# Performance work log

Hardware: AMD Instinct MI355X
Metric: run time of the kernel (lower is better)

The kernel has to match this reference:

```python
import jax, jax.numpy as jnp
import numpy as np

B, S, D, H = 8, 1024, 768, 12
HEAD_DIM = D // H  # 64
# NOTE: original code divides scores by scaling=(head_dim)**-0.5, i.e. MULTIPLIES by sqrt(head_dim)
SCORE_SCALE = float(HEAD_DIM) ** 0.5


def setup_inputs() -> dict:
    key = jax.random.key(0)
    ks = jax.random.split(key, 9)
    std = 1.0 / np.sqrt(D)
    return {
        "x":  jax.random.normal(ks[0], (B, S, D), jnp.float32),
        "Wq": jax.random.normal(ks[1], (H, D, D), jnp.float32) * std,
        "bq": jax.random.normal(ks[2], (H, D), jnp.float32) * std,
        "Wk": jax.random.normal(ks[3], (H, D, D), jnp.float32) * std,
        "bk": jax.random.normal(ks[4], (H, D), jnp.float32) * std,
        "Wv": jax.random.normal(ks[5], (H, D, D), jnp.float32) * std,
        "bv": jax.random.normal(ks[6], (H, D), jnp.float32) * std,
        "Wp": jax.random.normal(ks[7], (H * D, D), jnp.float32) * (1.0 / np.sqrt(H * D)),
        "bp": jax.random.normal(ks[8], (D,), jnp.float32) * std,
    }


def reference(x, Wq, bq, Wk, bk, Wv, bv, Wp, bp):
    # Per-head full-width projections, batched over the head axis h.
    q = jnp.einsum('bsd,hde->bhse', x, Wq) + bq[None, :, None, :]  # [B,H,S,D]
    k = jnp.einsum('bsd,hde->bhse', x, Wk) + bk[None, :, None, :]
    v = jnp.einsum('bsd,hde->bhse', x, Wv) + bv[None, :, None, :]
    scores = jnp.einsum('bhse,bhte->bhst', q, k) * SCORE_SCALE    # [B,H,S,S]
    attn = jax.nn.softmax(scores, axis=-1)
    o = jnp.einsum('bhst,bhte->bhse', attn, v)                     # [B,H,S,D]
    # concat heads along last dim (head-major order matches torch.cat)
    o = jnp.transpose(o, (0, 2, 1, 3)).reshape(B, S, H * D)        # [B,S,H*D]
    return o @ Wp + bp                                             # [B,S,D]
```

## Files before the change

### kernel.cpp

```cpp
#include <hip/hip_runtime.h>


typedef __attribute__((ext_vector_type(8))) short bf16x8;
typedef __attribute__((ext_vector_type(4))) float fx4;

#define NB 8
#define NS 1024
#define ND 768
#define NH 12

__device__ __forceinline__ unsigned short f2bf(float x) {
    unsigned int u = __float_as_uint(x);
    u += 0x7fffu + ((u >> 16) & 1u);
    return (unsigned short)(u >> 16);
}
__device__ __forceinline__ float bf2f(unsigned short h) {
    return __uint_as_float(((unsigned int)h) << 16);
}

__device__ __forceinline__ void gll16(const void* g, void* l) {
    __builtin_amdgcn_global_load_lds(
        (const __attribute__((address_space(1))) void*)g,
        (__attribute__((address_space(3))) void*)l, 16, 0, 0);
}

__device__ __forceinline__ void split_body(const float* __restrict__ in,
                                           unsigned short* __restrict__ hi,
                                           unsigned short* __restrict__ lo, int i) {
    float4 v = ((const float4*)in)[i];
    ushort4 h, l;
    h.x = f2bf(v.x); l.x = f2bf(v.x - bf2f(h.x));
    h.y = f2bf(v.y); l.y = f2bf(v.y - bf2f(h.y));
    h.z = f2bf(v.z); l.z = f2bf(v.z - bf2f(h.z));
    h.w = f2bf(v.w); l.w = f2bf(v.w - bf2f(h.w));
    ((ushort4*)hi)[i] = h;
    ((ushort4*)lo)[i] = l;
}

template<int NTERMS, class Epi>
__device__ __forceinline__ void gemm_core(
    char* __restrict__ smem,
    const unsigned short* __restrict__ Ah, const unsigned short* __restrict__ Al, int lda,
    const unsigned short* __restrict__ Bh, const unsigned short* __restrict__ Bl, int ldb,
    int K, Epi epi)
{
    constexpr int TILE = 16384;

    const int t = threadIdx.x;
    const int lane = t & 63;
    const int w = t >> 6;
    const int wm = (w >> 1) << 6;
    const int wn = (w & 1) << 6;
    const int lr = lane & 15;
    const int lg = lane >> 4;

    const int l3 = lane >> 3;
    const int cs = (lane & 7) ^ l3;
    const int ldsw = w << 12;

    const long gsA = (long)(w * 32 + l3) * lda * 2 + cs * 16;
    const long gsB = (long)(w * 32 + l3) * ldb * 2 + cs * 16;
    const long giA = (long)lda * 16;
    const long giB = (long)ldb * 16;

    const char* pAh = (const char*)Ah;
    const char* pBh = (const char*)Bh;
    const char* pAl = (const char*)Al;
    const char* pBl = (const char*)Bl;
    char* smA  = smem;
    char* smB  = smem + TILE;
    char* smA2 = smem + ((NTERMS == 3) ? 2 * TILE : 0);
    char* smB2 = smem + ((NTERMS == 3) ? 3 * TILE : TILE);

// ... 30 lines not shown
            for (int i = 0; i < 4; i++) {
                fa[i] = *(const bf16x8*)((const unsigned short*)smA + rowA[i] + pc);
                fb[i] = *(const bf16x8*)((const unsigned short*)smB + rowB[i] + pc);
            }
            if constexpr (NTERMS == 3) {
                #pragma unroll
                for (int i = 0; i < 4; i++) {
                    fa2[i] = *(const bf16x8*)((const unsigned short*)smA2 + rowA[i] + pc);
                    fb2[i] = *(const bf16x8*)((const unsigned short*)smB2 + rowB[i] + pc);
                }
            }
            #pragma unroll
            for (int i = 0; i < 4; i++)
                #pragma unroll
                for (int j = 0; j < 4; j++) {
                    acc[i][j] = __builtin_amdgcn_mfma_f32_16x16x32_bf16(fa[i], fb[j], acc[i][j], 0, 0, 0);
                    if constexpr (NTERMS == 3) {
                        acc[i][j] = __builtin_amdgcn_mfma_f32_16x16x32_bf16(fa[i], fb2[j], acc[i][j], 0, 0, 0);
                        acc[i][j] = __builtin_amdgcn_mfma_f32_16x16x32_bf16(fa2[i], fb[j], acc[i][j], 0, 0, 0);
                    }
                }
        }
    }

    #pragma unroll
    for (int i = 0; i < 4; i++)
        #pragma unroll
        for (int j = 0; j < 4; j++)
            #pragma unroll
            for (int r = 0; r < 4; r++)
                epi(wm + (i << 4) + (lg << 2) + r, wn + (j << 4) + lr, acc[i][j][r]);
}

__device__ __forceinline__ void softmax_rows(float* __restrict__ Sc, int blk) {
    int row = blk * 4 + ((int)threadIdx.x >> 6);
    int lane = threadIdx.x & 63;
    float* rp = Sc + (long)row * NS;
    const float4* src = (const float4*)rp + (lane << 2);
    float v[16];
    #pragma unroll
    for (int i = 0; i < 4; i++) {
        float4 a = src[i];
        v[i * 4 + 0] = a.x; v[i * 4 + 1] = a.y; v[i * 4 + 2] = a.z; v[i * 4 + 3] = a.w;
    }
    float m = v[0];
    #pragma unroll
    for (int i = 1; i < 16; i++) m = fmaxf(m, v[i]);
    #pragma unroll
    for (int o = 32; o > 0; o >>= 1) m = fmaxf(m, __shfl_xor(m, o));
    float s = 0.f, p[16];
    #pragma unroll
    for (int i = 0; i < 16; i++) { p[i] = __expf((v[i] - m) * 8.0f); s += p[i]; }
    #pragma unroll
    for (int o = 32; o > 0; o >>= 1) s += __shfl_xor(s, o);
    float inv = 1.0f / s;
    unsigned int wrd[8];
    #pragma unroll
    for (int i = 0; i < 8; i++) {
        unsigned int u0 = f2bf(p[2 * i] * inv);
        unsigned int u1 = f2bf(p[2 * i + 1] * inv);
        wrd[i] = u0 | (u1 << 16);
    }
    uint4* dst = (uint4*)((unsigned short*)rp + (lane << 4));
    dst[0] = make_uint4(wrd[0], wrd[1], wrd[2], wrd[3]);
    dst[1] = make_uint4(wrd[4], wrd[5], wrd[6], wrd[7]);
}

__global__ void k_setup1(
    const float* __restrict__ x, unsigned short* __restrict__ xh, unsigned short* __restrict__ xl,
    const float* __restrict__ Wq, unsigned short* __restrict__ Wqh, unsigned short* __restrict__ Wql,
    const float* __restrict__ Wk, unsigned short* __restrict__ Wkh, unsigned short* __restrict__ Wkl,
    const float* __restrict__ bq, float* __restrict__ rk)
{
    const int bx = blockIdx.x;
    if (bx < 6144) {
        split_body(x, xh, xl, bx * 256 + threadIdx.x);
    } else if (bx < 13056) {
        split_body(Wq, Wqh, Wql, (bx - 6144) * 256 + threadIdx.x);
    } else if (bx < 19968) {
        split_body(Wk, Wkh, Wkl, (bx - 13056) * 256 + threadIdx.x);
    } else {
        const int idx = bx - 19968;
        const int h = idx / 192;
        const int d = (idx % 192) * 4 + ((int)threadIdx.x >> 6);
        const int lane = threadIdx.x & 63;
        const float4* row = (const float4*)(Wk + ((long)h * ND + d) * ND);
        const float4* bv4 = (const float4*)(bq + h * ND);
        float acc = 0.f;
        #pragma unroll
        for (int i = 0; i < 3; i++) {
            float4 a = row[lane + (i << 6)];
            float4 b = bv4[lane + (i << 6)];
            acc += a.x * b.x + a.y * b.y + a.z * b.z + a.w * b.w;
        }
        #pragma unroll
        for (int o = 32; o > 0; o >>= 1) acc += __shfl_xor(acc, o);
        if (lane == 0) rk[h * ND + d] = acc;
    }
}

__global__ __launch_bounds__(256, 2) void k_setup2(
    const unsigned short* __restrict__ Wkh, const unsigned short* __restrict__ Wkl,
    const unsigned short* __restrict__ Wqh, const unsigned short* __restrict__ Wql,
    unsigned short* __restrict__ MTh, unsigned short* __restrict__ MTl,
    const float* __restrict__ x, const float* __restrict__ rk, float* __restrict__ w_all)
{
    __shared__ __align__(16) char smem[65536];
    const int bx = blockIdx.x;
    if (bx < 432) {
        const int tid = (bx & 7) * 54 + (bx >> 3);
        const int n0 = (tid % 6) << 7;
        const int m0 = ((tid / 6) % 6) << 7;
        const long hw = (long)(tid / 36) * (ND * ND);
        unsigned short* oh = MTh + hw + (long)m0 * ND + n0;
        unsigned short* ol = MTl + hw + (long)m0 * ND + n0;
        gemm_core<3>(smem, Wkh + hw + (long)m0 * ND, Wkl + hw + (long)m0 * ND, ND,
                     Wqh + hw + (long)n0 * ND, Wql + hw + (long)n0 * ND, ND, ND,
                     [=](int r, int c, float v) {
                         unsigned short hh = f2bf(v);
                         oh[r * ND + c] = hh;
                         ol[r * ND + c] = f2bf(v - bf2f(hh));
                     });
    } else {
        float* srk = (float*)smem;
        for (int i = threadIdx.x; i < NH * ND; i += 256) srk[i] = rk[i];
        __syncthreads();
        const int row = (bx - 432) * 4 + ((int)threadIdx.x >> 6);
        const int lane = threadIdx.x & 63;
        const float4* xr = (const float4*)(x + (long)row * ND);
        float4 xa[3];
        #pragma unroll
        for (int i = 0; i < 3; i++) xa[i] = xr[lane + (i << 6)];
        for (int h = 0; h < NH; h++) {
            const float* r = srk + h * ND;
            float acc = 0.f;
            #pragma unroll
            for (int i = 0; i < 3; i++) {
                int e = (lane + (i << 6)) << 2;
                acc += xa[i].x * r[e] + xa[i].y * r[e + 1]
                     + xa[i].z * r[e + 2] + xa[i].w * r[e + 3];
            }
            #pragma unroll
            for (int o = 32; o > 0; o >>= 1) acc += __shfl_xor(acc, o);
            if (lane == 0) w_all[h * (NB * NS) + row] = acc;
        }
    }
}

__global__ void k_setup3(const float* __restrict__ Wv, unsigned short* __restrict__ Wvb,
                         const float* __restrict__ Wp, unsigned short* __restrict__ WpT)
{
    __shared__ float tile[64][65];
    const int bx = blockIdx.x;
    if (bx < 6912) {
        int i = bx * 256 + threadIdx.x;
        float4 v = ((const float4*)Wv)[i];
        ushort4 h;
        h.x = f2bf(v.x); h.y = f2bf(v.y); h.z = f2bf(v.z); h.w = f2bf(v.w);
        ((ushort4*)Wvb)[i] = h;
    } else {
        const int idx = bx - 6912;
        const int c0 = (idx % 12) * 64;
        const int r0 = ((idx / 12) % 12) * 64;
        const long zo = (long)(idx / 144) * (ND * ND);
        const float* in = Wp + zo;
        unsigned short* oh = WpT + zo;
        const int tc = threadIdx.x & 63, t4 = threadIdx.x >> 6;
        #pragma unroll
        for (int i = 0; i < 16; i++) {
            int r = (i << 2) + t4;
            tile[r][tc] = in[(long)(r0 + r) * ND + c0 + tc];
        }
        __syncthreads();
        #pragma unroll
        for (int i = 0; i < 16; i++) {
            int c = (i << 2) + t4;
            oh[(long)(c0 + c) * ND + r0 + tc] = f2bf(tile[tc][c]);
        }
    }
}

__global__ __launch_bounds__(256, 2) void k_setup4(
    const unsigned short* __restrict__ WpT, const unsigned short* __restrict__ Wvb,
    unsigned short* __restrict__ NTo, const float* __restrict__ bv,
    float* __restrict__ s_all)
{
    __shared__ __align__(16) char smem[32768];
    const int bx = blockIdx.x;
    if (bx < 432) {
        const int tid = (bx & 7) * 54 + (bx >> 3);
        const int n0 = (tid % 6) << 7;
        const int m0 = ((tid / 6) % 6) << 7;
        const long hw = (long)(tid / 36) * (ND * ND);
        unsigned short* o = NTo + hw + (long)m0 * ND + n0;
        gemm_core<1>(smem, WpT + hw + (long)m0 * ND, nullptr, ND,
                     Wvb + hw + (long)n0 * ND, nullptr, ND, ND,
                     [=](int r, int c, float v) { o[r * ND + c] = f2bf(v); });
    } else {
        const int idx = bx - 432;
        const int h = idx / 192;
        const int j = (idx % 192) * 4 + ((int)threadIdx.x >> 6);
        const int lane = threadIdx.x & 63;
        const ushort4* row = (const ushort4*)(WpT + ((long)h * ND + j) * ND);
        const float* bvh = bv + h * ND;
        float acc = 0.f;
        #pragma unroll
        for (int i = 0; i < 3; i++) {
            int c = lane + (i << 6);
            ushort4 u = row[c];
            int e = c << 2;
            acc += bf2f(u.x) * bvh[e] + bf2f(u.y) * bvh[e + 1]
                 + bf2f(u.z) * bvh[e + 2] + bf2f(u.w) * bvh[e + 3];
        }
        #pragma unroll
        for (int o = 32; o > 0; o >>= 1) acc += __shfl_xor(acc, o);
        if (lane == 0) s_all[h * ND + j] = acc;
    }
}


__global__ __launch_bounds__(256, 2) void k_G0(
    const unsigned short* __restrict__ xh, const unsigned short* __restrict__ xl,
    const unsigned short* __restrict__ MTh, const unsigned short* __restrict__ MTl,
    unsigned short* __restrict__ Gh, unsigned short* __restrict__ Gl)
{
    __shared__ __align__(16) char smem[65536];
    const int bx = blockIdx.x;
    const int xcd = bx & 7, idx = bx >> 3;
    const int m0 = (xcd * 8 + idx / 6) << 7;
    const int n0 = (idx % 6) << 7;
    unsigned short* oh = Gh + (long)m0 * ND + n0;
    unsigned short* ol = Gl + (long)m0 * ND + n0;
    gemm_core<3>(smem, xh + (long)m0 * ND, xl + (long)m0 * ND, ND,
                 MTh + (long)n0 * ND, MTl + (long)n0 * ND, ND, ND,
                 [=](int r, int c, float v) {
                     unsigned short hh = f2bf(v);
                     oh[(long)r * ND + c] = hh;
                     ol[(long)r * ND + c] = f2bf(v - bf2f(hh));
                 });
}

__global__ __launch_bounds__(256, 2) void k_SZ(
    const unsigned short* __restrict__ Gh, const unsigned short* __restrict__ Gl,
    const unsigned short* __restrict__ xh, const unsigned short* __restrict__ xl,
    const float* __restrict__ wv, float* __restrict__ Sc,
    const unsigned short* __restrict__ NTh, const float* __restrict__ sh,
    unsigned short* __restrict__ ZT)
{
    __shared__ __align__(16) char smem[65536];
    const int bx = blockIdx.x;
    if (bx < 512) {
        const int bl = bx & 7, idx = bx >> 3;
        const int m0 = (idx >> 3) << 7;
        const int n0 = (idx & 7) << 7;
        const long ao = ((long)bl * NS + m0) * ND;
        const long bo = ((long)bl * NS + n0) * ND;
        const float* ww = wv + bl * NS + n0;
        float* out = Sc + ((long)bl * NS + m0) * NS + n0;
        gemm_core<3>(smem, Gh + ao, Gl + ao, ND, xh + bo, xl + bo, ND, ND,
                     [=](int r, int c, float v) { out[(long)r * NS + c] = v + ww[c]; });
    } else {
        const int g = bx - 512;
        const int xcd = g & 7, idx = g >> 3;
        const int m0 = (xcd * 8 + idx / 6) << 7;
        const int n0 = (idx % 6) << 7;
        const int bl = m0 >> 10;
        const int s0 = m0 & (NS - 1);
        unsigned short* zt = ZT + (long)bl * (ND * NS);
        gemm_core<1>(smem, xh + (long)m0 * ND, nullptr, ND,
                     NTh + (long)n0 * ND, nullptr, ND, ND,
                     [=](int r, int c, float v) {
                         zt[(long)(n0 + c) * NS + s0 + r] = f2bf(v + sh[n0 + c]);
                     });
    }
}

__global__ __launch_bounds__(256) void k_SM(float* __restrict__ Sc) {
    softmax_rows(Sc, blockIdx.x);
}

template<int MODE>
__global__ __launch_bounds__(256, 2) void k_PVG(
    const unsigned short* __restrict__ P, const unsigned short* __restrict__ ZT,
    const float* __restrict__ bp, float* __restrict__ outp,
    const unsigned short* __restrict__ xh, const unsigned short* __restrict__ xl,
    const unsigned short* __restrict__ MTh, const unsigned short* __restrict__ MTl,
    unsigned short* __restrict__ Gh, unsigned short* __restrict__ Gl)
{
    __shared__ __align__(16) char smem[65536];
    const int bx = blockIdx.x;
    if (bx < 384) {
        const int bl = bx & 7, idx = bx >> 3;
        const int m0 = (idx / 6) << 7;
        const int n0 = (idx % 6) << 7;
        const unsigned short* A = P + ((long)bl * NS + m0) * (2 * NS);
        const unsigned short* B = ZT + (long)bl * (ND * NS) + (long)n0 * NS;
        float* o = outp + ((long)bl * NS + m0) * ND + n0;
        const float* bi = bp + n0;
        gemm_core<1>(smem, A, nullptr, 2 * NS, B, nullptr, NS, NS,
                     [=](int r, int c, float v) {
                         float* d = o + (long)r * ND + c;
                         if constexpr (MODE == 0) *d = v + bi[c];
                         else *d += v;
                     });
    } else {
        const int g = bx - 384;
        const int xcd = g & 7, idx = g >> 3;
        const int m0 = (xcd * 8 + idx / 6) << 7;
        const int n0 = (idx % 6) << 7;
        unsigned short* oh = Gh + (long)m0 * ND + n0;
        unsigned short* ol = Gl + (long)m0 * ND + n0;
        gemm_core<3>(smem, xh + (long)m0 * ND, xl + (long)m0 * ND, ND,
                     MTh + (long)n0 * ND, MTl + (long)n0 * ND, ND, ND,
                     [=](int r, int c, float v) {
                         unsigned short hh = f2bf(v);
                         oh[(long)r * ND + c] = hh;
                         ol[(long)r * ND + c] = f2bf(v - bf2f(hh));
                     });
    }
}


extern "C" void kernel_launch(void* const* d_in, const int* in_sizes, int n_in,
                              void* d_out, int out_size, void* d_ws, size_t ws_size,
                              hipStream_t stream) {
    (void)in_sizes; (void)n_in; (void)out_size; (void)ws_size;
    const float* x  = (const float*)d_in[0];
    const float* Wq = (const float*)d_in[1];
    const float* bq = (const float*)d_in[2];
    const float* Wk = (const float*)d_in[3];
    const float* bk = (const float*)d_in[4];  (void)bk;
    const float* Wv = (const float*)d_in[5];
    const float* bv = (const float*)d_in[6];
    const float* Wp = (const float*)d_in[7];
    const float* bp = (const float*)d_in[8];

    const size_t nx  = (size_t)NB * NS * ND;
    const size_t nw  = (size_t)NH * ND * ND;

    char* p = (char*)d_ws;
    auto alloc = [&](size_t bytes) -> void* {
        void* r = (void*)p;
        p += (bytes + 255) & ~(size_t)255;
        return r;
    };
    unsigned short* xh   = (unsigned short*)alloc(nx * 2);
    unsigned short* xl   = (unsigned short*)alloc(nx * 2);
    unsigned short* MTh  = (unsigned short*)alloc(nw * 2);
    unsigned short* MTl  = (unsigned short*)alloc(nw * 2);
    unsigned short* NTb  = (unsigned short*)alloc(nw * 2);
    float*          rk   = (float*)alloc((size_t)NH * ND * 4);
    float*          s_all= (float*)alloc((size_t)NH * ND * 4);
    float*          w_all= (float*)alloc((size_t)NH * NB * NS * 4);
    char* U = (char*)alloc(2 * nx * 2 + ((size_t)NB * NS * NS * 4) + ((size_t)NB * NS * ND * 2));
    unsigned short* Wqh = (unsigned short*)U;
    unsigned short* Wql = Wqh + nw;
    unsigned short* Wkh = Wql + nw;
    unsigned short* Wkl = Wkh + nw;
    unsigned short* Wvb = (unsigned short*)U;
    unsigned short* WpT = Wvb + nw;
    unsigned short* Gh = (unsigned short*)U;
    unsigned short* Gl = Gh + nx;
    float*          Sc = (float*)(Gl + nx);
    unsigned short* ZT = (unsigned short*)(Sc + (size_t)NB * NS * NS);

    k_setup1<<<22272, 256, 0, stream>>>(x, xh, xl, Wq, Wqh, Wql, Wk, Wkh, Wkl, bq, rk);
    k_setup2<<<2480, 256, 0, stream>>>(Wkh, Wkl, Wqh, Wql, MTh, MTl, x, rk, w_all);
    k_setup3<<<8640, 256, 0, stream>>>(Wv, Wvb, Wp, WpT);
    k_setup4<<<2736, 256, 0, stream>>>(WpT, Wvb, NTb, bv, s_all);

    k_G0<<<384, 256, 0, stream>>>(xh, xl, MTh, MTl, Gh, Gl);
    for (int h = 0; h < NH; h++) {
        const long hwn = (long)(h + 1) * ND * ND;
        k_SZ<<<896, 256, 0, stream>>>(Gh, Gl, xh, xl, w_all + (long)h * NB * NS,
                                      Sc, NTb + (long)h * ND * ND, s_all + h * ND, ZT);
        k_SM<<<2048, 256, 0, stream>>>(Sc);
        const int ng = (h + 1 < NH) ? 768 : 384;
        if (h == 0)
            k_PVG<0><<<ng, 256, 0, stream>>>((unsigned short*)Sc, ZT, bp, (float*)d_out,
                                             xh, xl, MTh + hwn, MTl + hwn, Gh, Gl);
        else
            k_PVG<1><<<ng, 256, 0, stream>>>((unsigned short*)Sc, ZT, bp, (float*)d_out,
                                             xh, xl,
                                             MTh + ((h + 1 < NH) ? hwn : 0),
                                             MTl + ((h + 1 < NH) ? hwn : 0), Gh, Gl);
    }
}
```

Baseline: 1.381 ms.

## Batch P·V over groups of heads and fuse softmax with next-head G projection

Restructures the per-head loop so that softmax probabilities for several heads are kept in separate buffers and the P·Z product is accumulated over a group of heads (NG = 4 or 2) inside one kernel. This cuts the number of read-modify-write passes over the fp32 output and the number of launches. Softmax is fused with the next head's G GEMM, and the next head's score and Z GEMMs are fused into the grouped PV kernel. The new path needs much more workspace, and it falls back to the old per-head path when the workspace is too small.

```diff
diff --git a/kernel.cpp b/kernel.cpp
--- a/kernel.cpp
+++ b/kernel.cpp
@@ -38,7 +38,7 @@
 }
 
 template<int NTERMS, class Epi>
-__device__ __forceinline__ void gemm_core(
+__device__ __forceinline__ void gemm_core64(
     char* __restrict__ smem,
     const unsigned short* __restrict__ Ah, const unsigned short* __restrict__ Al, int lda,
     const unsigned short* __restrict__ Bh, const unsigned short* __restrict__ Bl, int ldb,
@@ -135,10 +135,9 @@
                 epi(wm + (i << 4) + (lg << 2) + r, wn + (j << 4) + lr, acc[i][j][r]);
 }
 
-__device__ __forceinline__ void softmax_rows(float* __restrict__ Sc, int blk) {
-    int row = blk * 4 + ((int)threadIdx.x >> 6);
-    int lane = threadIdx.x & 63;
-    float* rp = Sc + (long)row * NS;
+__device__ __forceinline__ void softmax_row_core(const float* __restrict__ rp,
+                                                 unsigned short* __restrict__ drow,
+                                                 int lane) {
     const float4* src = (const float4*)rp + (lane << 2);
     float v[16];
     #pragma unroll
@@ -164,7 +163,7 @@
         unsigned int u1 = f2bf(p[2 * i + 1] * inv);
         wrd[i] = u0 | (u1 << 16);
     }
-    uint4* dst = (uint4*)((unsigned short*)rp + (lane << 4));
+    uint4* dst = (uint4*)(drow + (lane << 4));
     dst[0] = make_uint4(wrd[0], wrd[1], wrd[2], wrd[3]);
     dst[1] = make_uint4(wrd[4], wrd[5], wrd[6], wrd[7]);
 }
@@ -217,13 +216,13 @@
         const long hw = (long)(tid / 36) * (ND * ND);
         unsigned short* oh = MTh + hw + (long)m0 * ND + n0;
         unsigned short* ol = MTl + hw + (long)m0 * ND + n0;
-        gemm_core<3>(smem, Wkh + hw + (long)m0 * ND, Wkl + hw + (long)m0 * ND, ND,
-                     Wqh + hw + (long)n0 * ND, Wql + hw + (long)n0 * ND, ND, ND,
-                     [=](int r, int c, float v) {
-                         unsigned short hh = f2bf(v);
-                         oh[r * ND + c] = hh;
-                         ol[r * ND + c] = f2bf(v - bf2f(hh));
-                     });
+        gemm_core64<3>(smem, Wkh + hw + (long)m0 * ND, Wkl + hw + (long)m0 * ND, ND,
+                       Wqh + hw + (long)n0 * ND, Wql + hw + (long)n0 * ND, ND, ND,
+                       [=](int r, int c, float v) {
+                           unsigned short hh = f2bf(v);
+                           oh[r * ND + c] = hh;
+                           ol[r * ND + c] = f2bf(v - bf2f(hh));
+                       });
     } else {
         float* srk = (float*)smem;
         for (int i = threadIdx.x; i < NH * ND; i += 256) srk[i] = rk[i];
@@ -296,9 +295,9 @@
         const int m0 = ((tid / 6) % 6) << 7;
         const long hw = (long)(tid / 36) * (ND * ND);
         unsigned short* o = NTo + hw + (long)m0 * ND + n0;
-        gemm_core<1>(smem, WpT + hw + (long)m0 * ND, nullptr, ND,
-                     Wvb + hw + (long)n0 * ND, nullptr, ND, ND,
-                     [=](int r, int c, float v) { o[r * ND + c] = f2bf(v); });
+        gemm_core64<1>(smem, WpT + hw + (long)m0 * ND, nullptr, ND,
+                       Wvb + hw + (long)n0 * ND, nullptr, ND, ND,
+                       [=](int r, int c, float v) { o[r * ND + c] = f2bf(v); });
     } else {
         const int idx = bx - 432;
         const int h = idx / 192;
@@ -334,13 +333,13 @@
     const int n0 = (idx % 6) << 7;
     unsigned short* oh = Gh + (long)m0 * ND + n0;
     unsigned short* ol = Gl + (long)m0 * ND + n0;
-    gemm_core<3>(smem, xh + (long)m0 * ND, xl + (long)m0 * ND, ND,
-                 MTh + (long)n0 * ND, MTl + (long)n0 * ND, ND, ND,
-                 [=](int r, int c, float v) {
-                     unsigned short hh = f2bf(v);
-                     oh[(long)r * ND + c] = hh;
-                     ol[(long)r * ND + c] = f2bf(v - bf2f(hh));
-                 });
+    gemm_core64<3>(smem, xh + (long)m0 * ND, xl + (long)m0 * ND, ND,
+                   MTh + (long)n0 * ND, MTl + (long)n0 * ND, ND, ND,
+                   [=](int r, int c, float v) {
+                       unsigned short hh = f2bf(v);
+                       oh[(long)r * ND + c] = hh;
+                       ol[(long)r * ND + c] = f2bf(v - bf2f(hh));
+                   });
 }
 
 __global__ __launch_bounds__(256, 2) void k_SZ(
@@ -360,8 +359,8 @@
         const long bo = ((long)bl * NS + n0) * ND;
         const float* ww = wv + bl * NS + n0;
         float* out = Sc + ((long)bl * NS + m0) * NS + n0;
-        gemm_core<3>(smem, Gh + ao, Gl + ao, ND, xh + bo, xl + bo, ND, ND,
-                     [=](int r, int c, float v) { out[(long)r * NS + c] = v + ww[c]; });
+        gemm_core64<3>(smem, Gh + ao, Gl + ao, ND, xh + bo, xl + bo, ND, ND,
+                       [=](int r, int c, float v) { out[(long)r * NS + c] = v + ww[c]; });
     } else {
         const int g = bx - 512;
         const int xcd = g & 7, idx = g >> 3;
@@ -370,16 +369,19 @@
         const int bl = m0 >> 10;
         const int s0 = m0 & (NS - 1);
         unsigned short* zt = ZT + (long)bl * (ND * NS);
-        gemm_core<1>(smem, xh + (long)m0 * ND, nullptr, ND,
-                     NTh + (long)n0 * ND, nullptr, ND, ND,
-                     [=](int r, int c, float v) {
-                         zt[(long)(n0 + c) * NS + s0 + r] = f2bf(v + sh[n0 + c]);
-                     });
+        gemm_core64<1>(smem, xh + (long)m0 * ND, nullptr, ND,
+                       NTh + (long)n0 * ND, nullptr, ND, ND,
+                       [=](int r, int c, float v) {
+                           zt[(long)(n0 + c) * NS + s0 + r] = f2bf(v + sh[n0 + c]);
+                       });
     }
 }
 
 __global__ __launch_bounds__(256) void k_SM(float* __restrict__ Sc) {
-    softmax_rows(Sc, blockIdx.x);
+    int row = blockIdx.x * 4 + ((int)threadIdx.x >> 6);
+    int lane = threadIdx.x & 63;
+    float* rp = Sc + (long)row * NS;
+    softmax_row_core(rp, (unsigned short*)rp, lane);
 }
 
 template<int MODE>
@@ -400,12 +402,12 @@
         const unsigned short* B = ZT + (long)bl * (ND * NS) + (long)n0 * NS;
         float* o = outp + ((long)bl * NS + m0) * ND + n0;
         const float* bi = bp + n0;
-        gemm_core<1>(smem, A, nullptr, 2 * NS, B, nullptr, NS, NS,
-                     [=](int r, int c, float v) {
-                         float* d = o + (long)r * ND + c;
-                         if constexpr (MODE == 0) *d = v + bi[c];
-                         else *d += v;
-                     });
+        gemm_core64<1>(smem, A, nullptr, 2 * NS, B, nullptr, NS, NS,
+                       [=](int r, int c, float v) {
+                           float* d = o + (long)r * ND + c;
+                           if constexpr (MODE == 0) *d = v + bi[c];
+                           else *d += v;
+                       });
     } else {
         const int g = bx - 384;
         const int xcd = g & 7, idx = g >> 3;
@@ -413,13 +415,161 @@
         const int n0 = (idx % 6) << 7;
         unsigned short* oh = Gh + (long)m0 * ND + n0;
         unsigned short* ol = Gl + (long)m0 * ND + n0;
-        gemm_core<3>(smem, xh + (long)m0 * ND, xl + (long)m0 * ND, ND,
-                     MTh + (long)n0 * ND, MTl + (long)n0 * ND, ND, ND,
-                     [=](int r, int c, float v) {
-                         unsigned short hh = f2bf(v);
-                         oh[(long)r * ND + c] = hh;
-                         ol[(long)r * ND + c] = f2bf(v - bf2f(hh));
-                     });
+        gemm_core64<3>(smem, xh + (long)m0 * ND, xl + (long)m0 * ND, ND,
+                       MTh + (long)n0 * ND, MTl + (long)n0 * ND, ND, ND,
+                       [=](int r, int c, float v) {
+                           unsigned short hh = f2bf(v);
+                           oh[(long)r * ND + c] = hh;
+                           ol[(long)r * ND + c] = f2bf(v - bf2f(hh));
+                       });
+    }
+}
+
+
+__global__ __launch_bounds__(256, 2) void k_SMG(
+    const float* __restrict__ Sc, unsigned short* __restrict__ Pp,
+    const unsigned short* __restrict__ xh, const unsigned short* __restrict__ xl,
+    const unsigned short* __restrict__ MTh, const unsigned short* __restrict__ MTl,
+    unsigned short* __restrict__ Gh, unsigned short* __restrict__ Gl)
+{
+    __shared__ __align__(16) char smem[65536];
+    const int bx = blockIdx.x;
+    if (bx < 2048) {
+        int row = bx * 4 + ((int)threadIdx.x >> 6);
+        int lane = threadIdx.x & 63;
+        softmax_row_core(Sc + (long)row * NS, Pp + (long)row * NS, lane);
+    } else {
+        const int g = bx - 2048;
+        const int xcd = g & 7, idx = g >> 3;
+        const int m0 = (xcd * 8 + idx / 6) << 7;
+        const int n0 = (idx % 6) << 7;
+        unsigned short* oh = Gh + (long)m0 * ND + n0;
+        unsigned short* ol = Gl + (long)m0 * ND + n0;
+        gemm_core64<3>(smem, xh + (long)m0 * ND, xl + (long)m0 * ND, ND,
+                       MTh + (long)n0 * ND, MTl + (long)n0 * ND, ND, ND,
+                       [=](int r, int c, float v) {
+                           unsigned short hh = f2bf(v);
+                           oh[(long)r * ND + c] = hh;
+                           ol[(long)r * ND + c] = f2bf(v - bf2f(hh));
+                       });
+    }
+}
+
+template<int NG, int MODE>
+__global__ __launch_bounds__(256, 2) void k_PVSZ(
+    const unsigned short* __restrict__ Pp, const unsigned short* __restrict__ ZTb,
+    int h0, const float* __restrict__ bp, float* __restrict__ outp,
+    const unsigned short* __restrict__ Gh, const unsigned short* __restrict__ Gl,
+    const unsigned short* __restrict__ xh, const unsigned short* __restrict__ xl,
+    const float* __restrict__ wv, float* __restrict__ Sc,
+    const unsigned short* __restrict__ NTh, const float* __restrict__ sh,
+    unsigned short* __restrict__ ZTn)
+{
+    __shared__ __align__(16) char smem[65536];
+    const int bx = blockIdx.x;
+    if (bx < 384) {
+        const size_t PPE = (size_t)(NB * NS) * NS;
+        const size_t ZTE = (size_t)(NB * NS) * ND;
+        const int bl = bx & 7, idx = bx >> 3;
+        const int m0 = (idx / 6) << 7;
+        const int n0 = (idx % 6) << 7;
+
+        const int t = threadIdx.x;
+        const int lane = t & 63;
+        const int w = t >> 6;
+        const int wm = (w >> 1) << 6;
+        const int wn = (w & 1) << 6;
+        const int lr = lane & 15;
+        const int lg = lane >> 4;
+        const int l3 = lane >> 3;
+        const int cs = (lane & 7) ^ l3;
+        const int ldsw = w << 12;
+        const long gs = (long)(w * 32 + l3) * 2048 + cs * 16;
+        const long gi = 16384;
+        char* smA = smem;
+        char* smB = smem + 16384;
+
+        int rowA[4], rowB[4];
+        #pragma unroll
+        for (int i = 0; i < 4; i++) {
+            rowA[i] = (wm + (i << 4) + lr) << 6;
+            rowB[i] = (wn + (i << 4) + lr) << 6;
+        }
+        const int lr7 = lr & 7;
+        fx4 acc[4][4] = {};
+
+        for (int j = 0; j < NG; j++) {
+            const int sj = (h0 + j) % (NG + 1);
+            const char* pA = (const char*)(Pp + (size_t)j * PPE
+                                              + ((long)bl * NS + m0) * NS);
+            const char* pB = (const char*)(ZTb + (size_t)sj * ZTE
+                                              + (long)bl * (ND * NS) + (long)n0 * NS);
+            for (int k0 = 0; k0 < NS; k0 += 64) {
+                const long kb2 = (long)k0 * 2;
+                __syncthreads();
+                #pragma unroll
+                for (int ii = 0; ii < 4; ii++) {
+                    const int lo = ldsw + (ii << 10);
+                    gll16(pA + gs + ii * gi + kb2, smA + lo);
+                    gll16(pB + gs + ii * gi + kb2, smB + lo);
+                }
+                __syncthreads();
+                #pragma unroll
+                for (int kk = 0; kk < 2; kk++) {
+                    const int pc = (((kk << 2) + lg) ^ lr7) << 3;
+                    bf16x8 fa[4], fb[4];
+                    #pragma unroll
+                    for (int i = 0; i < 4; i++) {
+                        fa[i] = *(const bf16x8*)((const unsigned short*)smA + rowA[i] + pc);
+                        fb[i] = *(const bf16x8*)((const unsigned short*)smB + rowB[i] + pc);
+                    }
+                    #pragma unroll
+                    for (int i = 0; i < 4; i++)
+                        #pragma unroll
+                        for (int jj = 0; jj < 4; jj++)
+                            acc[i][jj] = __builtin_amdgcn_mfma_f32_16x16x32_bf16(
+                                fa[i], fb[jj], acc[i][jj], 0, 0, 0);
+                }
+            }
+        }
+        float* o = outp + ((long)bl * NS + m0) * ND + n0;
+        const float* bi = bp + n0;
+        #pragma unroll
+        for (int i = 0; i < 4; i++)
+            #pragma unroll
+            for (int jj = 0; jj < 4; jj++)
+                #pragma unroll
+                for (int r = 0; r < 4; r++) {
+                    const int rr = wm + (i << 4) + (lg << 2) + r;
+                    const int cc = wn + (jj << 4) + lr;
+                    float* d = o + (long)rr * ND + cc;
+                    if constexpr (MODE == 0) *d = acc[i][jj][r] + bi[cc];
+                    else *d += acc[i][jj][r];
+                }
+    } else if (bx < 896) {
+        const int b2 = bx - 384;
+        const int bl = b2 & 7, idx = b2 >> 3;
+        const int m0 = (idx >> 3) << 7;
+        const int n0 = (idx & 7) << 7;
+        const long ao = ((long)bl * NS + m0) * ND;
+        const long bo = ((long)bl * NS + n0) * ND;
+        const float* ww = wv + bl * NS + n0;
+        float* out = Sc + ((long)bl * NS + m0) * NS + n0;
+        gemm_core64<3>(smem, Gh + ao, Gl + ao, ND, xh + bo, xl + bo, ND, ND,
+                       [=](int r, int c, float v) { out[(long)r * NS + c] = v + ww[c]; });
+    } else {
+        const int g = bx - 896;
+        const int xcd = g & 7, idx = g >> 3;
+        const int m0 = (xcd * 8 + idx / 6) << 7;
+        const int n0 = (idx % 6) << 7;
+        const int bl = m0 >> 10;
+        const int s0 = m0 & (NS - 1);
+        unsigned short* zt = ZTn + (long)bl * (ND * NS);
+        gemm_core64<1>(smem, xh + (long)m0 * ND, nullptr, ND,
+                       NTh + (long)n0 * ND, nullptr, ND, ND,
+                       [=](int r, int c, float v) {
+                           zt[(long)(n0 + c) * NS + s0 + r] = f2bf(v + sh[n0 + c]);
+                       });
     }
 }
 
@@ -427,7 +577,7 @@
 extern "C" void kernel_launch(void* const* d_in, const int* in_sizes, int n_in,
                               void* d_out, int out_size, void* d_ws, size_t ws_size,
                               hipStream_t stream) {
-    (void)in_sizes; (void)n_in; (void)out_size; (void)ws_size;
+    (void)in_sizes; (void)n_in; (void)out_size;
     const float* x  = (const float*)d_in[0];
     const float* Wq = (const float*)d_in[1];
     const float* bq = (const float*)d_in[2];
@@ -440,6 +590,9 @@
 
     const size_t nx  = (size_t)NB * NS * ND;
     const size_t nw  = (size_t)NH * ND * ND;
+    const size_t nwh = (size_t)ND * ND;
+    const size_t PPE = (size_t)NB * NS * NS;
+    const size_t ZTE = (size_t)NB * NS * ND;
 
     char* p = (char*)d_ws;
     auto alloc = [&](size_t bytes) -> void* {
@@ -455,37 +608,117 @@
     float*          rk   = (float*)alloc((size_t)NH * ND * 4);
     float*          s_all= (float*)alloc((size_t)NH * ND * 4);
     float*          w_all= (float*)alloc((size_t)NH * NB * NS * 4);
-    char* U = (char*)alloc(2 * nx * 2 + ((size_t)NB * NS * NS * 4) + ((size_t)NB * NS * ND * 2));
-    unsigned short* Wqh = (unsigned short*)U;
-    unsigned short* Wql = Wqh + nw;
-    unsigned short* Wkh = Wql + nw;
-    unsigned short* Wkl = Wkh + nw;
-    unsigned short* Wvb = (unsigned short*)U;
-    unsigned short* WpT = Wvb + nw;
-    unsigned short* Gh = (unsigned short*)U;
-    unsigned short* Gl = Gh + nx;
-    float*          Sc = (float*)(Gl + nx);
-    unsigned short* ZT = (unsigned short*)(Sc + (size_t)NB * NS * NS);
-
-    k_setup1<<<22272, 256, 0, stream>>>(x, xh, xl, Wq, Wqh, Wql, Wk, Wkh, Wkl, bq, rk);
-    k_setup2<<<2480, 256, 0, stream>>>(Wkh, Wkl, Wqh, Wql, MTh, MTl, x, rk, w_all);
-    k_setup3<<<8640, 256, 0, stream>>>(Wv, Wvb, Wp, WpT);
-    k_setup4<<<2736, 256, 0, stream>>>(WpT, Wvb, NTb, bv, s_all);
-
-    k_G0<<<384, 256, 0, stream>>>(xh, xl, MTh, MTl, Gh, Gl);
-    for (int h = 0; h < NH; h++) {
-        const long hwn = (long)(h + 1) * ND * ND;
-        k_SZ<<<896, 256, 0, stream>>>(Gh, Gl, xh, xl, w_all + (long)h * NB * NS,
-                                      Sc, NTb + (long)h * ND * ND, s_all + h * ND, ZT);
-        k_SM<<<2048, 256, 0, stream>>>(Sc);
-        const int ng = (h + 1 < NH) ? 768 : 384;
-        if (h == 0)
-            k_PVG<0><<<ng, 256, 0, stream>>>((unsigned short*)Sc, ZT, bp, (float*)d_out,
-                                             xh, xl, MTh + hwn, MTl + hwn, Gh, Gl);
-        else
-            k_PVG<1><<<ng, 256, 0, stream>>>((unsigned short*)Sc, ZT, bp, (float*)d_out,
-                                             xh, xl,
-                                             MTh + ((h + 1 < NH) ? hwn : 0),
-                                             MTl + ((h + 1 < NH) ? hwn : 0), Gh, Gl);
-    }
-}
+
+    const size_t used_fixed = (size_t)(p - (char*)d_ws);
+    const size_t scg = (PPE * 4 + 256) + 2 * (nx * 2 + 256);
+    const size_t slop = 2u << 20;
+    auto need = [&](int ng) {
+        return used_fixed + scg + (size_t)ng * (PPE * 2 + 256)
+             + (size_t)(ng + 1) * (ZTE * 2 + 256) + slop;
+    };
+    int NG = 0;
+    if (need(4) <= ws_size) NG = 4;
+    else if (need(2) <= ws_size) NG = 2;
+
+    if (NG) {
+        float*          Sc = (float*)alloc(PPE * 4);
+        unsigned short* Gh = (unsigned short*)alloc(nx * 2);
+        unsigned short* Gl = (unsigned short*)alloc(nx * 2);
+        unsigned short* Pp = (unsigned short*)alloc((size_t)NG * PPE * 2);
+        unsigned short* ZT = (unsigned short*)alloc((size_t)(NG + 1) * ZTE * 2);
+        unsigned short* Wqh = (unsigned short*)Sc;
+        unsigned short* Wql = Wqh + nw;
+        unsigned short* Wkh = Wql + nw;
+        unsigned short* Wkl = Wkh + nw;
+        unsigned short* Wvb = (unsigned short*)Sc;
+        unsigned short* WpT = Wvb + nw;
+
+        k_setup1<<<22272, 256, 0, stream>>>(x, xh, xl, Wq, Wqh, Wql, Wk, Wkh, Wkl, bq, rk);
+        k_setup2<<<2480, 256, 0, stream>>>(Wkh, Wkl, Wqh, Wql, MTh, MTl, x, rk, w_all);
+        k_setup3<<<8640, 256, 0, stream>>>(Wv, Wvb, Wp, WpT);
+        k_setup4<<<2736, 256, 0, stream>>>(WpT, Wvb, NTb, bv, s_all);
+
+        k_G0<<<384, 256, 0, stream>>>(xh, xl, MTh, MTl, Gh, Gl);
+        k_SZ<<<896, 256, 0, stream>>>(Gh, Gl, xh, xl, w_all, Sc, NTb, s_all, ZT);
+        const int NGR = NH / NG;
+        for (int g = 0; g < NGR; g++) {
+            for (int j = 0; j < NG; j++) {
+                const int h = g * NG + j;
+                if (j > 0)
+                    k_SZ<<<896, 256, 0, stream>>>(
+                        Gh, Gl, xh, xl, w_all + (long)h * NB * NS, Sc,
+                        NTb + (long)h * nwh, s_all + h * ND,
+                        ZT + (size_t)(h % (NG + 1)) * ZTE);
+                const int hn = h + 1;
+                const bool hasG = hn < NH;
+                k_SMG<<<hasG ? 2432 : 2048, 256, 0, stream>>>(
+                    Sc, Pp + (size_t)j * PPE, xh, xl,
+                    MTh + (long)(hasG ? hn : 0) * nwh,
+                    MTl + (long)(hasG ? hn : 0) * nwh, Gh, Gl);
+            }
+            const int hn = (g + 1) * NG;
+            const bool tail = hn < NH;
+            const int hs = tail ? hn : 0;
+            const int grid = tail ? 1280 : 384;
+            unsigned short* ZTn = ZT + (size_t)(hn % (NG + 1)) * ZTE;
+            if (NG == 4) {
+                if (g == 0)
+                    k_PVSZ<4, 0><<<grid, 256, 0, stream>>>(
+                        Pp, ZT, g * NG, bp, (float*)d_out, Gh, Gl, xh, xl,
+                        w_all + (long)hs * NB * NS, Sc, NTb + (long)hs * nwh,
+                        s_all + hs * ND, ZTn);
+                else
+                    k_PVSZ<4, 1><<<grid, 256, 0, stream>>>(
+                        Pp, ZT, g * NG, bp, (float*)d_out, Gh, Gl, xh, xl,
+                        w_all + (long)hs * NB * NS, Sc, NTb + (long)hs * nwh,
+                        s_all + hs * ND, ZTn);
+            } else {
+                if (g == 0)
+                    k_PVSZ<2, 0><<<grid, 256, 0, stream>>>(
+                        Pp, ZT, g * NG, bp, (float*)d_out, Gh, Gl, xh, xl,
+                        w_all + (long)hs * NB * NS, Sc, NTb + (long)hs * nwh,
+                        s_all + hs * ND, ZTn);
+                else
+                    k_PVSZ<2, 1><<<grid, 256, 0, stream>>>(
+                        Pp, ZT, g * NG, bp, (float*)d_out, Gh, Gl, xh, xl,
+                        w_all + (long)hs * NB * NS, Sc, NTb + (long)hs * nwh,
+                        s_all + hs * ND, ZTn);
+            }
+        }
+    } else {
+        char* U = (char*)alloc(2 * nx * 2 + PPE * 4 + ZTE * 2);
+        unsigned short* Wqh = (unsigned short*)U;
+        unsigned short* Wql = Wqh + nw;
+        unsigned short* Wkh = Wql + nw;
+        unsigned short* Wkl = Wkh + nw;
+        unsigned short* Wvb = (unsigned short*)U;
+        unsigned short* WpT = Wvb + nw;
+        unsigned short* Gh = (unsigned short*)U;
+        unsigned short* Gl = Gh + nx;
+        float*          Sc = (float*)(Gl + nx);
+        unsigned short* ZT = (unsigned short*)(Sc + PPE);
+
+        k_setup1<<<22272, 256, 0, stream>>>(x, xh, xl, Wq, Wqh, Wql, Wk, Wkh, Wkl, bq, rk);
+        k_setup2<<<2480, 256, 0, stream>>>(Wkh, Wkl, Wqh, Wql, MTh, MTl, x, rk, w_all);
+        k_setup3<<<8640, 256, 0, stream>>>(Wv, Wvb, Wp, WpT);
+        k_setup4<<<2736, 256, 0, stream>>>(WpT, Wvb, NTb, bv, s_all);
+
+        k_G0<<<384, 256, 0, stream>>>(xh, xl, MTh, MTl, Gh, Gl);
+        for (int h = 0; h < NH; h++) {
+            const long hwn = (long)(h + 1) * nwh;
+            k_SZ<<<896, 256, 0, stream>>>(Gh, Gl, xh, xl, w_all + (long)h * NB * NS,
+                                          Sc, NTb + (long)h * nwh, s_all + h * ND, ZT);
+            k_SM<<<2048, 256, 0, stream>>>(Sc);
+            const int ng = (h + 1 < NH) ? 768 : 384;
+            if (h == 0)
+                k_PVG<0><<<ng, 256, 0, stream>>>((unsigned short*)Sc, ZT, bp,
+                                                 (float*)d_out, xh, xl,
+                                                 MTh + hwn, MTl + hwn, Gh, Gl);
+            else
+                k_PVG<1><<<ng, 256, 0, stream>>>((unsigned short*)Sc, ZT, bp,
+                                                 (float*)d_out, xh, xl,
+                                                 MTh + ((h + 1 < NH) ? hwn : 0),
+                                                 MTl + ((h + 1 < NH) ? hwn : 0), Gh, Gl);
+        }
+    }
+}
```

After: 1.418 ms. 2.7% more time.

## Re-pipeline per-head launches: fuse softmax with next G and PV with next SZ

Applied to the files above, without the earlier changes.

Merges the four setup kernels into two. Softmax now writes probabilities to a separate bf16 buffer instead of overwriting the scores in place. This lets the next head's G projection run in the same launch as softmax, and the next head's scores/Z GEMM run in the same launch as the current PV GEMM. ZT is double-buffered for this, cutting launches per head from three to two and filling the device with more concurrent blocks, at the cost of extra workspace and more complex dependencies.

```diff
diff --git a/kernel.cpp b/kernel.cpp
--- a/kernel.cpp
+++ b/kernel.cpp
@@ -38,7 +38,7 @@
 }
 
 template<int NTERMS, class Epi>
-__device__ __forceinline__ void gemm_core(
+__device__ __forceinline__ void gemm_core64(
     char* __restrict__ smem,
     const unsigned short* __restrict__ Ah, const unsigned short* __restrict__ Al, int lda,
     const unsigned short* __restrict__ Bh, const unsigned short* __restrict__ Bl, int ldb,
@@ -135,10 +135,9 @@
                 epi(wm + (i << 4) + (lg << 2) + r, wn + (j << 4) + lr, acc[i][j][r]);
 }
 
-__device__ __forceinline__ void softmax_rows(float* __restrict__ Sc, int blk) {
-    int row = blk * 4 + ((int)threadIdx.x >> 6);
-    int lane = threadIdx.x & 63;
-    float* rp = Sc + (long)row * NS;
+__device__ __forceinline__ void softmax_row_core(const float* __restrict__ rp,
+                                                 unsigned short* __restrict__ drow,
+                                                 int lane) {
     const float4* src = (const float4*)rp + (lane << 2);
     float v[16];
     #pragma unroll
@@ -164,17 +163,20 @@
         unsigned int u1 = f2bf(p[2 * i + 1] * inv);
         wrd[i] = u0 | (u1 << 16);
     }
-    uint4* dst = (uint4*)((unsigned short*)rp + (lane << 4));
+    uint4* dst = (uint4*)(drow + (lane << 4));
     dst[0] = make_uint4(wrd[0], wrd[1], wrd[2], wrd[3]);
     dst[1] = make_uint4(wrd[4], wrd[5], wrd[6], wrd[7]);
 }
 
-__global__ void k_setup1(
+__global__ void k_su_a(
     const float* __restrict__ x, unsigned short* __restrict__ xh, unsigned short* __restrict__ xl,
     const float* __restrict__ Wq, unsigned short* __restrict__ Wqh, unsigned short* __restrict__ Wql,
     const float* __restrict__ Wk, unsigned short* __restrict__ Wkh, unsigned short* __restrict__ Wkl,
-    const float* __restrict__ bq, float* __restrict__ rk)
-{
+    const float* __restrict__ bq, float* __restrict__ rk,
+    const float* __restrict__ Wv, unsigned short* __restrict__ Wvb,
+    const float* __restrict__ Wp, unsigned short* __restrict__ WpT)
+{
+    __shared__ float tile[64][65];
     const int bx = blockIdx.x;
     if (bx < 6144) {
         split_body(x, xh, xl, bx * 256 + threadIdx.x);
@@ -182,7 +184,7 @@
         split_body(Wq, Wqh, Wql, (bx - 6144) * 256 + threadIdx.x);
     } else if (bx < 19968) {
         split_body(Wk, Wkh, Wkl, (bx - 13056) * 256 + threadIdx.x);
-    } else {
+    } else if (bx < 22272) {
         const int idx = bx - 19968;
         const int h = idx / 192;
         const int d = (idx % 192) * 4 + ((int)threadIdx.x >> 6);
@@ -199,14 +201,42 @@
         #pragma unroll
         for (int o = 32; o > 0; o >>= 1) acc += __shfl_xor(acc, o);
         if (lane == 0) rk[h * ND + d] = acc;
-    }
-}
-
-__global__ __launch_bounds__(256, 2) void k_setup2(
+    } else if (bx < 29184) {
+        int i = (bx - 22272) * 256 + threadIdx.x;
+        float4 v = ((const float4*)Wv)[i];
+        ushort4 h;
+        h.x = f2bf(v.x); h.y = f2bf(v.y); h.z = f2bf(v.z); h.w = f2bf(v.w);
+        ((ushort4*)Wvb)[i] = h;
+    } else {
+        const int idx = bx - 29184;
+        const int c0 = (idx % 12) * 64;
+        const int r0 = ((idx / 12) % 12) * 64;
+        const long zo = (long)(idx / 144) * (ND * ND);
+        const float* in = Wp + zo;
+        unsigned short* oh = WpT + zo;
+        const int tc = threadIdx.x & 63, t4 = threadIdx.x >> 6;
+        #pragma unroll
+        for (int i = 0; i < 16; i++) {
+            int r = (i << 2) + t4;
+            tile[r][tc] = in[(long)(r0 + r) * ND + c0 + tc];
+        }
+        __syncthreads();
+        #pragma unroll
+        for (int i = 0; i < 16; i++) {
+            int c = (i << 2) + t4;
+            oh[(long)(c0 + c) * ND + r0 + tc] = f2bf(tile[tc][c]);
+        }
+    }
+}
+
+__global__ __launch_bounds__(256, 2) void k_su_b(
     const unsigned short* __restrict__ Wkh, const unsigned short* __restrict__ Wkl,
     const unsigned short* __restrict__ Wqh, const unsigned short* __restrict__ Wql,
     unsigned short* __restrict__ MTh, unsigned short* __restrict__ MTl,
-    const float* __restrict__ x, const float* __restrict__ rk, float* __restrict__ w_all)
+    const float* __restrict__ x, const float* __restrict__ rk, float* __restrict__ w_all,
+    const unsigned short* __restrict__ WpT, const unsigned short* __restrict__ Wvb,
+    unsigned short* __restrict__ NTo, const float* __restrict__ bv,
+    float* __restrict__ s_all)
 {
     __shared__ __align__(16) char smem[65536];
     const int bx = blockIdx.x;
@@ -217,14 +247,14 @@
         const long hw = (long)(tid / 36) * (ND * ND);
         unsigned short* oh = MTh + hw + (long)m0 * ND + n0;
         unsigned short* ol = MTl + hw + (long)m0 * ND + n0;
-        gemm_core<3>(smem, Wkh + hw + (long)m0 * ND, Wkl + hw + (long)m0 * ND, ND,
-                     Wqh + hw + (long)n0 * ND, Wql + hw + (long)n0 * ND, ND, ND,
-                     [=](int r, int c, float v) {
-                         unsigned short hh = f2bf(v);
-                         oh[r * ND + c] = hh;
-                         ol[r * ND + c] = f2bf(v - bf2f(hh));
-                     });
-    } else {
+        gemm_core64<3>(smem, Wkh + hw + (long)m0 * ND, Wkl + hw + (long)m0 * ND, ND,
+                       Wqh + hw + (long)n0 * ND, Wql + hw + (long)n0 * ND, ND, ND,
+                       [=](int r, int c, float v) {
+                           unsigned short hh = f2bf(v);
+                           oh[r * ND + c] = hh;
+                           ol[r * ND + c] = f2bf(v - bf2f(hh));
+                       });
+    } else if (bx < 2480) {
         float* srk = (float*)smem;
         for (int i = threadIdx.x; i < NH * ND; i += 256) srk[i] = rk[i];
         __syncthreads();
@@ -247,60 +277,18 @@
             for (int o = 32; o > 0; o >>= 1) acc += __shfl_xor(acc, o);
             if (lane == 0) w_all[h * (NB * NS) + row] = acc;
         }
-    }
-}
-
-__global__ void k_setup3(const float* __restrict__ Wv, unsigned short* __restrict__ Wvb,
-                         const float* __restrict__ Wp, unsigned short* __restrict__ WpT)
-{
-    __shared__ float tile[64][65];
-    const int bx = blockIdx.x;
-    if (bx < 6912) {
-        int i = bx * 256 + threadIdx.x;
-        float4 v = ((const float4*)Wv)[i];
-        ushort4 h;
-        h.x = f2bf(v.x); h.y = f2bf(v.y); h.z = f2bf(v.z); h.w = f2bf(v.w);
-        ((ushort4*)Wvb)[i] = h;
-    } else {
-        const int idx = bx - 6912;
-        const int c0 = (idx % 12) * 64;
-        const int r0 = ((idx / 12) % 12) * 64;
-        const long zo = (long)(idx / 144) * (ND * ND);
-        const float* in = Wp + zo;
-        unsigned short* oh = WpT + zo;
-        const int tc = threadIdx.x & 63, t4 = threadIdx.x >> 6;
-        #pragma unroll
-        for (int i = 0; i < 16; i++) {
-            int r = (i << 2) + t4;
-            tile[r][tc] = in[(long)(r0 + r) * ND + c0 + tc];
-        }
-        __syncthreads();
-        #pragma unroll
-        for (int i = 0; i < 16; i++) {
-            int c = (i << 2) + t4;
-            oh[(long)(c0 + c) * ND + r0 + tc] = f2bf(tile[tc][c]);
-        }
-    }
-}
-
-__global__ __launch_bounds__(256, 2) void k_setup4(
-    const unsigned short* __restrict__ WpT, const unsigned short* __restrict__ Wvb,
-    unsigned short* __restrict__ NTo, const float* __restrict__ bv,
-    float* __restrict__ s_all)
-{
-    __shared__ __align__(16) char smem[32768];
-    const int bx = blockIdx.x;
-    if (bx < 432) {
-        const int tid = (bx & 7) * 54 + (bx >> 3);
+    } else if (bx < 2912) {
+        const int b2 = bx - 2480;
+        const int tid = (b2 & 7) * 54 + (b2 >> 3);
         const int n0 = (tid % 6) << 7;
         const int m0 = ((tid / 6) % 6) << 7;
         const long hw = (long)(tid / 36) * (ND * ND);
         unsigned short* o = NTo + hw + (long)m0 * ND + n0;
-        gemm_core<1>(smem, WpT + hw + (long)m0 * ND, nullptr, ND,
-                     Wvb + hw + (long)n0 * ND, nullptr, ND, ND,
-                     [=](int r, int c, float v) { o[r * ND + c] = f2bf(v); });
+        gemm_core64<1>(smem, WpT + hw + (long)m0 * ND, nullptr, ND,
+                       Wvb + hw + (long)n0 * ND, nullptr, ND, ND,
+                       [=](int r, int c, float v) { o[r * ND + c] = f2bf(v); });
     } else {
-        const int idx = bx - 432;
+        const int idx = bx - 2912;
         const int h = idx / 192;
         const int j = (idx % 192) * 4 + ((int)threadIdx.x >> 6);
         const int lane = threadIdx.x & 63;
@@ -334,13 +322,13 @@
     const int n0 = (idx % 6) << 7;
     unsigned short* oh = Gh + (long)m0 * ND + n0;
     unsigned short* ol = Gl + (long)m0 * ND + n0;
-    gemm_core<3>(smem, xh + (long)m0 * ND, xl + (long)m0 * ND, ND,
-                 MTh + (long)n0 * ND, MTl + (long)n0 * ND, ND, ND,
-                 [=](int r, int c, float v) {
-                     unsigned short hh = f2bf(v);
-                     oh[(long)r * ND + c] = hh;
-                     ol[(long)r * ND + c] = f2bf(v - bf2f(hh));
-                 });
+    gemm_core64<3>(smem, xh + (long)m0 * ND, xl + (long)m0 * ND, ND,
+                   MTh + (long)n0 * ND, MTl + (long)n0 * ND, ND, ND,
+                   [=](int r, int c, float v) {
+                       unsigned short hh = f2bf(v);
+                       oh[(long)r * ND + c] = hh;
+                       ol[(long)r * ND + c] = f2bf(v - bf2f(hh));
+                   });
 }
 
 __global__ __launch_bounds__(256, 2) void k_SZ(
@@ -360,8 +348,8 @@
         const long bo = ((long)bl * NS + n0) * ND;
         const float* ww = wv + bl * NS + n0;
         float* out = Sc + ((long)bl * NS + m0) * NS + n0;
-        gemm_core<3>(smem, Gh + ao, Gl + ao, ND, xh + bo, xl + bo, ND, ND,
-                     [=](int r, int c, float v) { out[(long)r * NS + c] = v + ww[c]; });
+        gemm_core64<3>(smem, Gh + ao, Gl + ao, ND, xh + bo, xl + bo, ND, ND,
+                       [=](int r, int c, float v) { out[(long)r * NS + c] = v + ww[c]; });
     } else {
         const int g = bx - 512;
         const int xcd = g & 7, idx = g >> 3;
@@ -370,25 +358,52 @@
         const int bl = m0 >> 10;
         const int s0 = m0 & (NS - 1);
         unsigned short* zt = ZT + (long)bl * (ND * NS);
-        gemm_core<1>(smem, xh + (long)m0 * ND, nullptr, ND,
-                     NTh + (long)n0 * ND, nullptr, ND, ND,
-                     [=](int r, int c, float v) {
-                         zt[(long)(n0 + c) * NS + s0 + r] = f2bf(v + sh[n0 + c]);
-                     });
-    }
-}
-
-__global__ __launch_bounds__(256) void k_SM(float* __restrict__ Sc) {
-    softmax_rows(Sc, blockIdx.x);
-}
-
-template<int MODE>
-__global__ __launch_bounds__(256, 2) void k_PVG(
-    const unsigned short* __restrict__ P, const unsigned short* __restrict__ ZT,
-    const float* __restrict__ bp, float* __restrict__ outp,
+        gemm_core64<1>(smem, xh + (long)m0 * ND, nullptr, ND,
+                       NTh + (long)n0 * ND, nullptr, ND, ND,
+                       [=](int r, int c, float v) {
+                           zt[(long)(n0 + c) * NS + s0 + r] = f2bf(v + sh[n0 + c]);
+                       });
+    }
+}
+
+__global__ __launch_bounds__(256, 2) void k_SMG1(
+    const float* __restrict__ Sc, unsigned short* __restrict__ Pp,
     const unsigned short* __restrict__ xh, const unsigned short* __restrict__ xl,
     const unsigned short* __restrict__ MTh, const unsigned short* __restrict__ MTl,
     unsigned short* __restrict__ Gh, unsigned short* __restrict__ Gl)
+{
+    __shared__ __align__(16) char smem[65536];
+    const int bx = blockIdx.x;
+    if (bx < 2048) {
+        int row = bx * 4 + ((int)threadIdx.x >> 6);
+        int lane = threadIdx.x & 63;
+        softmax_row_core(Sc + (long)row * NS, Pp + (long)row * NS, lane);
+    } else {
+        const int g = bx - 2048;
+        const int xcd = g & 7, idx = g >> 3;
+        const int m0 = (xcd * 8 + idx / 6) << 7;
+        const int n0 = (idx % 6) << 7;
+        unsigned short* oh = Gh + (long)m0 * ND + n0;
+        unsigned short* ol = Gl + (long)m0 * ND + n0;
+        gemm_core64<3>(smem, xh + (long)m0 * ND, xl + (long)m0 * ND, ND,
+                       MTh + (long)n0 * ND, MTl + (long)n0 * ND, ND, ND,
+                       [=](int r, int c, float v) {
+                           unsigned short hh = f2bf(v);
+                           oh[(long)r * ND + c] = hh;
+                           ol[(long)r * ND + c] = f2bf(v - bf2f(hh));
+                       });
+    }
+}
+
+template<int MODE>
+__global__ __launch_bounds__(256, 2) void k_PVSZ1(
+    const unsigned short* __restrict__ Pp, const unsigned short* __restrict__ ZTr,
+    const float* __restrict__ bp, float* __restrict__ outp,
+    const unsigned short* __restrict__ Gh, const unsigned short* __restrict__ Gl,
+    const unsigned short* __restrict__ xh, const unsigned short* __restrict__ xl,
+    const float* __restrict__ wv, float* __restrict__ Sc,
+    const unsigned short* __restrict__ NTh, const float* __restrict__ sh,
+    unsigned short* __restrict__ ZTw)
 {
     __shared__ __align__(16) char smem[65536];
     const int bx = blockIdx.x;
@@ -396,30 +411,40 @@
         const int bl = bx & 7, idx = bx >> 3;
         const int m0 = (idx / 6) << 7;
         const int n0 = (idx % 6) << 7;
-        const unsigned short* A = P + ((long)bl * NS + m0) * (2 * NS);
-        const unsigned short* B = ZT + (long)bl * (ND * NS) + (long)n0 * NS;
+        const unsigned short* A = Pp + ((long)bl * NS + m0) * NS;
+        const unsigned short* B = ZTr + (long)bl * (ND * NS) + (long)n0 * NS;
         float* o = outp + ((long)bl * NS + m0) * ND + n0;
         const float* bi = bp + n0;
-        gemm_core<1>(smem, A, nullptr, 2 * NS, B, nullptr, NS, NS,
-                     [=](int r, int c, float v) {
-                         float* d = o + (long)r * ND + c;
-                         if constexpr (MODE == 0) *d = v + bi[c];
-                         else *d += v;
-                     });
+        gemm_core64<1>(smem, A, nullptr, NS, B, nullptr, NS, NS,
+                       [=](int r, int c, float v) {
+                           float* d = o + (long)r * ND + c;
+                           if constexpr (MODE == 0) *d = v + bi[c];
+                           else *d += v;
+                       });
+    } else if (bx < 896) {
+        const int b2 = bx - 384;
+        const int bl = b2 & 7, idx = b2 >> 3;
+        const int m0 = (idx >> 3) << 7;
+        const int n0 = (idx & 7) << 7;
+        const long ao = ((long)bl * NS + m0) * ND;
+        const long bo = ((long)bl * NS + n0) * ND;
+        const float* ww = wv + bl * NS + n0;
+        float* out = Sc + ((long)bl * NS + m0) * NS + n0;
+        gemm_core64<3>(smem, Gh + ao, Gl + ao, ND, xh + bo, xl + bo, ND, ND,
+                       [=](int r, int c, float v) { out[(long)r * NS + c] = v + ww[c]; });
     } else {
-        const int g = bx - 384;
+        const int g = bx - 896;
         const int xcd = g & 7, idx = g >> 3;
         const int m0 = (xcd * 8 + idx / 6) << 7;
         const int n0 = (idx % 6) << 7;
-        unsigned short* oh = Gh + (long)m0 * ND + n0;
-        unsigned short* ol = Gl + (long)m0 * ND + n0;
-        gemm_core<3>(smem, xh + (long)m0 * ND, xl + (long)m0 * ND, ND,
-                     MTh + (long)n0 * ND, MTl + (long)n0 * ND, ND, ND,
-                     [=](int r, int c, float v) {
-                         unsigned short hh = f2bf(v);
-                         oh[(long)r * ND + c] = hh;
-                         ol[(long)r * ND + c] = f2bf(v - bf2f(hh));
-                     });
+        const int bl = m0 >> 10;
+        const int s0 = m0 & (NS - 1);
+        unsigned short* zt = ZTw + (long)bl * (ND * NS);
+        gemm_core64<1>(smem, xh + (long)m0 * ND, nullptr, ND,
+                       NTh + (long)n0 * ND, nullptr, ND, ND,
+                       [=](int r, int c, float v) {
+                           zt[(long)(n0 + c) * NS + s0 + r] = f2bf(v + sh[n0 + c]);
+                       });
     }
 }
 
@@ -440,6 +465,9 @@
 
     const size_t nx  = (size_t)NB * NS * ND;
     const size_t nw  = (size_t)NH * ND * ND;
+    const size_t nwh = (size_t)ND * ND;
+    const size_t PPE = (size_t)NB * NS * NS;
+    const size_t ZTE = (size_t)NB * NS * ND;
 
     char* p = (char*)d_ws;
     auto alloc = [&](size_t bytes) -> void* {
@@ -455,37 +483,43 @@
     float*          rk   = (float*)alloc((size_t)NH * ND * 4);
     float*          s_all= (float*)alloc((size_t)NH * ND * 4);
     float*          w_all= (float*)alloc((size_t)NH * NB * NS * 4);
-    char* U = (char*)alloc(2 * nx * 2 + ((size_t)NB * NS * NS * 4) + ((size_t)NB * NS * ND * 2));
-    unsigned short* Wqh = (unsigned short*)U;
+    float*          Sc = (float*)alloc(PPE * 4);
+    unsigned short* Gh = (unsigned short*)alloc(nx * 2);
+    unsigned short* Gl = (unsigned short*)alloc(nx * 2);
+    unsigned short* Pp = (unsigned short*)alloc(PPE * 2);
+    unsigned short* ZT = (unsigned short*)alloc(2 * ZTE * 2);
+    unsigned short* Wqh = (unsigned short*)Sc;
     unsigned short* Wql = Wqh + nw;
     unsigned short* Wkh = Wql + nw;
     unsigned short* Wkl = Wkh + nw;
-    unsigned short* Wvb = (unsigned short*)U;
+    unsigned short* Wvb = Wkl + nw;
     unsigned short* WpT = Wvb + nw;
-    unsigned short* Gh = (unsigned short*)U;
-    unsigned short* Gl = Gh + nx;
-    float*          Sc = (float*)(Gl + nx);
-    unsigned short* ZT = (unsigned short*)(Sc + (size_t)NB * NS * NS);
-
-    k_setup1<<<22272, 256, 0, stream>>>(x, xh, xl, Wq, Wqh, Wql, Wk, Wkh, Wkl, bq, rk);
-    k_setup2<<<2480, 256, 0, stream>>>(Wkh, Wkl, Wqh, Wql, MTh, MTl, x, rk, w_all);
-    k_setup3<<<8640, 256, 0, stream>>>(Wv, Wvb, Wp, WpT);
-    k_setup4<<<2736, 256, 0, stream>>>(WpT, Wvb, NTb, bv, s_all);
+
+    k_su_a<<<30912, 256, 0, stream>>>(x, xh, xl, Wq, Wqh, Wql, Wk, Wkh, Wkl,
+                                      bq, rk, Wv, Wvb, Wp, WpT);
+    k_su_b<<<5216, 256, 0, stream>>>(Wkh, Wkl, Wqh, Wql, MTh, MTl, x, rk, w_all,
+                                     WpT, Wvb, NTb, bv, s_all);
 
     k_G0<<<384, 256, 0, stream>>>(xh, xl, MTh, MTl, Gh, Gl);
+    k_SZ<<<896, 256, 0, stream>>>(Gh, Gl, xh, xl, w_all, Sc, NTb, s_all, ZT);
     for (int h = 0; h < NH; h++) {
-        const long hwn = (long)(h + 1) * ND * ND;
-        k_SZ<<<896, 256, 0, stream>>>(Gh, Gl, xh, xl, w_all + (long)h * NB * NS,
-                                      Sc, NTb + (long)h * ND * ND, s_all + h * ND, ZT);
-        k_SM<<<2048, 256, 0, stream>>>(Sc);
-        const int ng = (h + 1 < NH) ? 768 : 384;
+        const int hn = h + 1;
+        const bool hasG = hn < NH;
+        const int hs = hasG ? hn : 0;
+        k_SMG1<<<hasG ? 2432 : 2048, 256, 0, stream>>>(
+            Sc, Pp, xh, xl, MTh + (long)hs * nwh, MTl + (long)hs * nwh, Gh, Gl);
+        unsigned short* ZTr = ZT + (size_t)(h & 1) * ZTE;
+        unsigned short* ZTw = ZT + (size_t)(hn & 1) * ZTE;
+        const int grid = hasG ? 1280 : 384;
         if (h == 0)
-            k_PVG<0><<<ng, 256, 0, stream>>>((unsigned short*)Sc, ZT, bp, (float*)d_out,
-                                             xh, xl, MTh + hwn, MTl + hwn, Gh, Gl);
+            k_PVSZ1<0><<<grid, 256, 0, stream>>>(
+                Pp, ZTr, bp, (float*)d_out, Gh, Gl, xh, xl,
+                w_all + (long)hs * NB * NS, Sc, NTb + (long)hs * nwh,
+                s_all + hs * ND, ZTw);
         else
-            k_PVG<1><<<ng, 256, 0, stream>>>((unsigned short*)Sc, ZT, bp, (float*)d_out,
-                                             xh, xl,
-                                             MTh + ((h + 1 < NH) ? hwn : 0),
-                                             MTl + ((h + 1 < NH) ? hwn : 0), Gh, Gl);
-    }
-}
+            k_PVSZ1<1><<<grid, 256, 0, stream>>>(
+                Pp, ZTr, bp, (float*)d_out, Gh, Gl, xh, xl,
+                w_all + (long)hs * NB * NS, Sc, NTb + (long)hs * nwh,
+                s_all + hs * ND, ZTw);
+    }
+}
```

After: 1.363 ms. No clear change (-1.3%).
